# Optimization experiments

Hardware: AMD Instinct MI355X
Metric: run time of the kernel (lower is better)

## Reference

```python
import jax, jax.numpy as jnp
import numpy as np

ROI = 31            # roi_size (odd)
HALF = ROI // 2     # tf.cast(roi_size/2, int32) == 15


def setup_inputs() -> dict:
    key = jax.random.key(0)
    k1, k2, k3, k4 = jax.random.split(key, 4)
    B, H, W, C, N = 16, 256, 256, 32, 4096
    encoded_poses = jax.random.normal(k1, (B, H, W, C), dtype=jnp.float32)
    b = jax.random.randint(k2, (N, 1), 0, B)
    y = jax.random.randint(k3, (N, 1), 0, H)
    x = jax.random.randint(k4, (N, 1), 0, W)
    roi_centers = jnp.concatenate([b, y, x], axis=1).astype(jnp.int32)
    return {"encoded_poses": encoded_poses, "roi_centers": roi_centers}


def reference(encoded_poses, roi_centers):
    # encoded_poses: [B, H, W, C]; roi_centers: [N, 3] = (batch, y, x)
    H, W = encoded_poses.shape[1], encoded_poses.shape[2]
    off = jnp.arange(ROI, dtype=roi_centers.dtype) - HALF          # [ROI]
    b = roi_centers[:, 0]                                          # [N]
    rows = roi_centers[:, 1, None] + off                           # [N, ROI]
    cols = roi_centers[:, 2, None] + off                           # [N, ROI]
    # Out-of-bounds positions get zero padding (as in tf.pad of the original).
    rmask = (rows >= 0) & (rows < H)
    cmask = (cols >= 0) & (cols < W)
    rc = jnp.clip(rows, 0, H - 1)
    cc = jnp.clip(cols, 0, W - 1)
    # Batched gather: [N, ROI, ROI, C]
    cuts = encoded_poses[b[:, None, None], rc[:, :, None], cc[:, None, :], :]
    mask = (rmask[:, :, None] & cmask[:, None, :])[..., None]
    return jnp.where(mask, cuts, jnp.zeros((), dtype=cuts.dtype))
```

## Files before the change

### kernel.cpp

```cpp
#include <hip/hip_runtime.h>

#define ROI 31
#define HALF 15
#define H_DIM 256
#define W_DIM 256
#define C_DIM 32
#define NSTRIP (16 * H_DIM)
#define CAP 96

typedef float vfloat4 __attribute__((ext_vector_type(4)));

__global__ __launch_bounds__(1024) void init_counts_kernel(int* __restrict__ counts) {
    const int i = blockIdx.x * 1024 + threadIdx.x;
    if (i < NSTRIP) counts[i] = 0;
}

__global__ __launch_bounds__(256) void build_lists_kernel(
    const int* __restrict__ centers, int* __restrict__ counts,
    int* __restrict__ lists, int N)
{
    const int n = blockIdx.x * 256 + threadIdx.x;
    if (n >= N) return;
    const int b = centers[3 * n + 0];
    const int y = centers[3 * n + 1];
    const int r0 = max(y - HALF, 0), r1 = min(y + HALF, H_DIM - 1);
    for (int rr = r0; rr <= r1; ++rr) {
        const int strip = (b << 8) | rr;
        const int pos = atomicAdd(&counts[strip], 1);
        if (pos < CAP) lists[strip * CAP + pos] = n;
    }
}

__global__ __launch_bounds__(256) void strip_scatter_kernel(
    const float* __restrict__ poses, const int* __restrict__ centers,
    const int* __restrict__ counts, const int* __restrict__ lists,
    float* __restrict__ out)
{
    __shared__ vfloat4 row_lds[W_DIM * C_DIM / 4];

    const int strip = blockIdx.x;
    const int b  = strip >> 8;
    const int rr = strip & (H_DIM - 1);
    const int t  = threadIdx.x;

    const vfloat4* src_row = reinterpret_cast<const vfloat4*>(
        poses + ((size_t)b * H_DIM + rr) * W_DIM * C_DIM);
    #pragma unroll
    for (int i = 0; i < 8; ++i)
        row_lds[i * 256 + t] = src_row[i * 256 + t];
    __syncthreads();

    const int cnt = min(counts[strip], CAP);
    const int pc = t >> 3;
    const int q  = t & 7;
    if (pc >= ROI) return;

    for (int j = 0; j < cnt; ++j) {
        const int n = lists[strip * CAP + j];
        const int y = centers[3 * n + 1];
        const int x = centers[3 * n + 2];
        const int c0 = max(x - HALF, 0), c1 = min(x + HALF, W_DIM - 1);
        const int nc = c1 - c0 + 1;
        const int r  = rr - (y - HALF);
        if (pc < nc) {
            const int cc = c0 + pc;
            const int oc = cc - (x - HALF);
            vfloat4 v = row_lds[cc * 8 + q];
            float* dst = out + (((size_t)n * ROI + r) * ROI + oc) * C_DIM + q * 4;
            __builtin_nontemporal_store(v, reinterpret_cast<vfloat4*>(dst));
        }
    }
}

__global__ __launch_bounds__(256) void zero_oob_kernel(
    const int* __restrict__ centers, float* __restrict__ out)
{
    const int n = blockIdx.x;
    const int y = centers[3 * n + 1];
    const int x = centers[3 * n + 2];
    if (y >= HALF && y <= H_DIM - 1 - HALF && x >= HALF && x <= W_DIM - 1 - HALF)
        return;

    const int t = threadIdx.x;
    if (t >= ROI * (C_DIM / 4)) return;
    const int c = t >> 3;
    const int q = t & 7;
    const int cc = x + c - HALF;
    const bool cok = (cc >= 0) && (cc < W_DIM);

    const vfloat4 z = (vfloat4)0.0f;
    for (int r = 0; r < ROI; ++r) {
        const int rr = y + r - HALF;
        const bool ok = cok && (rr >= 0) && (rr < H_DIM);
        if (!ok) {
            vfloat4* dst = reinterpret_cast<vfloat4*>(
                out + (((size_t)n * ROI + r) * ROI + c) * C_DIM) + q;
            __builtin_nontemporal_store(z, dst);
        }
    }
}

extern "C" void kernel_launch(void* const* d_in, const int* in_sizes, int n_in,
                              void* d_out, int out_size, void* d_ws, size_t ws_size,
                              hipStream_t stream) {
    const float* poses   = (const float*)d_in[0];
    const int*   centers = (const int*)d_in[1];
    float*       out     = (float*)d_out;

    int* counts = (int*)d_ws;
    int* lists  = counts + NSTRIP;

    const int N = in_sizes[1] / 3;

    init_counts_kernel<<<dim3((NSTRIP + 1023) / 1024), dim3(1024), 0, stream>>>(counts);
    build_lists_kernel<<<dim3((N + 255) / 256), dim3(256), 0, stream>>>(centers, counts, lists, N);
    strip_scatter_kernel<<<dim3(NSTRIP), dim3(256), 0, stream>>>(poses, centers, counts, lists, out);
    zero_oob_kernel<<<dim3(N), dim3(256), 0, stream>>>(centers, out);
}
```

Measured before the change: 137.8 us.

## Replace per-strip atomic lists with single-block counting sort by (batch,row)

```diff
diff --git a/kernel.cpp b/kernel.cpp
--- a/kernel.cpp
+++ b/kernel.cpp
@@ -5,35 +5,61 @@
 #define H_DIM 256
 #define W_DIM 256
 #define C_DIM 32
-#define NSTRIP (16 * H_DIM)
-#define CAP 96
+#define NBKT 4096
 
 typedef float vfloat4 __attribute__((ext_vector_type(4)));
 
-__global__ __launch_bounds__(1024) void init_counts_kernel(int* __restrict__ counts) {
-    const int i = blockIdx.x * 1024 + threadIdx.x;
-    if (i < NSTRIP) counts[i] = 0;
-}
+__global__ __launch_bounds__(1024) void sort_kernel(
+    const int* __restrict__ centers, int* __restrict__ perm,
+    int* __restrict__ off, int N)
+{
+    __shared__ int hist[NBKT];
+    __shared__ int base[NBKT];
+    __shared__ int partial[1024];
+    const int t = threadIdx.x;
 
-__global__ __launch_bounds__(256) void build_lists_kernel(
-    const int* __restrict__ centers, int* __restrict__ counts,
-    int* __restrict__ lists, int N)
-{
-    const int n = blockIdx.x * 256 + threadIdx.x;
-    if (n >= N) return;
-    const int b = centers[3 * n + 0];
-    const int y = centers[3 * n + 1];
-    const int r0 = max(y - HALF, 0), r1 = min(y + HALF, H_DIM - 1);
-    for (int rr = r0; rr <= r1; ++rr) {
-        const int strip = (b << 8) | rr;
-        const int pos = atomicAdd(&counts[strip], 1);
-        if (pos < CAP) lists[strip * CAP + pos] = n;
+    for (int k = t; k < NBKT; k += 1024) hist[k] = 0;
+    __syncthreads();
+
+    for (int i = t; i < N; i += 1024) {
+        const int key = (centers[3 * i] << 8) | centers[3 * i + 1];
+        atomicAdd(&hist[key], 1);
+    }
+    __syncthreads();
+
+    const int s0 = hist[4 * t], s1 = hist[4 * t + 1];
+    const int s2 = hist[4 * t + 2], s3 = hist[4 * t + 3];
+    const int loc = s0 + s1 + s2 + s3;
+    partial[t] = loc;
+    __syncthreads();
+    for (int o = 1; o < 1024; o <<= 1) {
+        int v = (t >= o) ? partial[t - o] : 0;
+        __syncthreads();
+        partial[t] += v;
+        __syncthreads();
+    }
+    const int ex = partial[t] - loc;
+    base[4 * t]     = ex;
+    base[4 * t + 1] = ex + s0;
+    base[4 * t + 2] = ex + s0 + s1;
+    base[4 * t + 3] = ex + s0 + s1 + s2;
+    __syncthreads();
+
+    for (int k = t; k < NBKT; k += 1024) off[k] = base[k];
+    if (t == 0) off[NBKT] = N;
+    for (int k = t; k < NBKT; k += 1024) hist[k] = 0;
+    __syncthreads();
+
+    for (int i = t; i < N; i += 1024) {
+        const int key = (centers[3 * i] << 8) | centers[3 * i + 1];
+        const int pos = base[key] + atomicAdd(&hist[key], 1);
+        perm[pos] = i;
     }
 }
 
 __global__ __launch_bounds__(256) void strip_scatter_kernel(
     const float* __restrict__ poses, const int* __restrict__ centers,
-    const int* __restrict__ counts, const int* __restrict__ lists,
+    const int* __restrict__ perm, const int* __restrict__ off,
     float* __restrict__ out)
 {
     __shared__ vfloat4 row_lds[W_DIM * C_DIM / 4];
@@ -50,53 +76,49 @@
         row_lds[i * 256 + t] = src_row[i * 256 + t];
     __syncthreads();
 
-    const int cnt = min(counts[strip], CAP);
+    const int ylo = max(rr - HALF, 0), yhi = min(rr + HALF, H_DIM - 1);
+    const int start = off[(b << 8) | ylo];
+    const int end   = off[((b << 8) | yhi) + 1];
+
     const int pc = t >> 3;
     const int q  = t & 7;
     if (pc >= ROI) return;
 
-    for (int j = 0; j < cnt; ++j) {
-        const int n = lists[strip * CAP + j];
+    for (int pos = start; pos < end; ++pos) {
+        const int n = perm[pos];
         const int y = centers[3 * n + 1];
         const int x = centers[3 * n + 2];
-        const int c0 = max(x - HALF, 0), c1 = min(x + HALF, W_DIM - 1);
-        const int nc = c1 - c0 + 1;
         const int r  = rr - (y - HALF);
-        if (pc < nc) {
-            const int cc = c0 + pc;
-            const int oc = cc - (x - HALF);
-            vfloat4 v = row_lds[cc * 8 + q];
-            float* dst = out + (((size_t)n * ROI + r) * ROI + oc) * C_DIM + q * 4;
-            __builtin_nontemporal_store(v, reinterpret_cast<vfloat4*>(dst));
-        }
+        const int cc = x - HALF + pc;
+        const bool cok = (cc >= 0) && (cc < W_DIM);
+        const int ccc = min(max(cc, 0), W_DIM - 1);
+        vfloat4 v = cok ? row_lds[ccc * 8 + q] : (vfloat4)0.0f;
+        float* dst = out + (((size_t)n * ROI + r) * ROI + pc) * C_DIM + q * 4;
+        __builtin_nontemporal_store(v, reinterpret_cast<vfloat4*>(dst));
     }
 }
 
-__global__ __launch_bounds__(256) void zero_oob_kernel(
+__global__ __launch_bounds__(256) void zero_rows_kernel(
     const int* __restrict__ centers, float* __restrict__ out)
 {
     const int n = blockIdx.x;
     const int y = centers[3 * n + 1];
-    const int x = centers[3 * n + 2];
-    if (y >= HALF && y <= H_DIM - 1 - HALF && x >= HALF && x <= W_DIM - 1 - HALF)
-        return;
-
+    if (y >= HALF && y <= H_DIM - 1 + HALF - ROI + 1) {  }
     const int t = threadIdx.x;
     if (t >= ROI * (C_DIM / 4)) return;
-    const int c = t >> 3;
-    const int q = t & 7;
-    const int cc = x + c - HALF;
-    const bool cok = (cc >= 0) && (cc < W_DIM);
+    const int pc = t >> 3;
+    const int q  = t & 7;
+    const vfloat4 z = (vfloat4)0.0f;
 
-    const vfloat4 z = (vfloat4)0.0f;
-    for (int r = 0; r < ROI; ++r) {
-        const int rr = y + r - HALF;
-        const bool ok = cok && (rr >= 0) && (rr < H_DIM);
-        if (!ok) {
-            vfloat4* dst = reinterpret_cast<vfloat4*>(
-                out + (((size_t)n * ROI + r) * ROI + c) * C_DIM) + q;
-            __builtin_nontemporal_store(z, dst);
-        }
+    const int rlo_end   = max(HALF - y, 0);
+    const int rhi_start = min(H_DIM - 1 + HALF - y + 1, ROI);
+    for (int r = 0; r < rlo_end; ++r) {
+        float* dst = out + (((size_t)n * ROI + r) * ROI + pc) * C_DIM + q * 4;
+        __builtin_nontemporal_store(z, reinterpret_cast<vfloat4*>(dst));
+    }
+    for (int r = rhi_start; r < ROI; ++r) {
+        float* dst = out + (((size_t)n * ROI + r) * ROI + pc) * C_DIM + q * 4;
+        __builtin_nontemporal_store(z, reinterpret_cast<vfloat4*>(dst));
     }
 }
 
@@ -107,13 +129,13 @@
     const int*   centers = (const int*)d_in[1];
     float*       out     = (float*)d_out;
 
-    int* counts = (int*)d_ws;
-    int* lists  = counts + NSTRIP;
+    const int N = in_sizes[1] / 3;
+    const int B = in_sizes[0] / (H_DIM * W_DIM * C_DIM);
 
-    const int N = in_sizes[1] / 3;
+    int* perm = (int*)d_ws;
+    int* off  = perm + N;
 
-    init_counts_kernel<<<dim3((NSTRIP + 1023) / 1024), dim3(1024), 0, stream>>>(counts);
-    build_lists_kernel<<<dim3((N + 255) / 256), dim3(256), 0, stream>>>(centers, counts, lists, N);
-    strip_scatter_kernel<<<dim3(NSTRIP), dim3(256), 0, stream>>>(poses, centers, counts, lists, out);
-    zero_oob_kernel<<<dim3(N), dim3(256), 0, stream>>>(centers, out);
+    sort_kernel<<<dim3(1), dim3(1024), 0, stream>>>(centers, perm, off, N);
+    strip_scatter_kernel<<<dim3(B * H_DIM), dim3(256), 0, stream>>>(poses, centers, perm, off, out);
+    zero_rows_kernel<<<dim3(N), dim3(256), 0, stream>>>(centers, out);
 }
```

New measurement: 116.4 us. -15.5%, faster.
